# Kernel tuning notes

Measured on AMD Instinct MI355X. Metric: run time of the kernel, lower is better.

## Reference

```python
import jax, jax.numpy as jnp
import numpy as np

H = 1024  # hidden_size
B, S = 64, 2048


def setup_inputs() -> dict:
    key = jax.random.key(0)
    ks = jax.random.split(key, 9)
    d = {
        "s_t": jax.random.normal(ks[0], (B, 2 * H), jnp.float32),
        "h_i": jax.random.normal(ks[1], (B, S, 2 * H), jnp.float32),
        "coverage": jax.random.uniform(ks[2], (B, S), jnp.float32),
        # parameters (torch Linear: y = x @ W.T + b)
        "W_h": jax.random.normal(ks[3], (H, 2 * H), jnp.float32) / np.sqrt(2 * H),
        "b_h": jnp.zeros((H,), jnp.float32),
        "W_s": jax.random.normal(ks[4], (H, 2 * H), jnp.float32) / np.sqrt(2 * H),
        "b_s": jnp.zeros((H,), jnp.float32),
        "W_c": jax.random.normal(ks[5], (H, 1), jnp.float32),  # no bias
        "v_a": jax.random.normal(ks[6], (1, H), jnp.float32) / np.sqrt(H),
        "b_a": jnp.zeros((1,), jnp.float32),
    }
    return d


def reference(s_t, h_i, coverage, W_h, b_h, W_s, b_s, W_c, v_a, b_a):
    # Wi_hi: (B,S,H)
    Wi_hi = jnp.einsum("bsd,hd->bsh", h_i, W_h) + b_h
    # Ws_s: (B,H)
    Ws_s = jnp.einsum("bd,hd->bh", s_t, W_s) + b_s
    # coverage features: (B,S,H)  (W_c is (H,1))
    cov_feat = coverage[:, :, None] * W_c[:, 0]
    # scores: (B,S)
    E = jnp.einsum("bsh,h->bs", jnp.tanh(Wi_hi + Ws_s[:, None, :] + cov_feat), v_a[0]) + b_a[0]
    A = jax.nn.softmax(E, axis=-1)
    # context: (B,2H)
    C = jnp.einsum("bs,bsd->bd", A, h_i)
    new_cov = coverage + A
    return (C, A, new_cov)
```

## Files before the change

kernel.cpp:

```cpp
#include <hip/hip_runtime.h>
#include <hip/hip_bf16.h>

typedef __bf16 bf16x8_v __attribute__((ext_vector_type(8)));
typedef float  f32x4_v  __attribute__((ext_vector_type(4)));

static constexpr int kH = 1024;
static constexpr int kD = 2048;
static constexpr int kB = 64;
static constexpr int kS = 2048;
static constexpr int kM = kB * kS;

__device__ __forceinline__ void load_lds16(const void* g, void* l) {
  __builtin_amdgcn_global_load_lds(
      (const __attribute__((address_space(1))) unsigned int*)g,
      (__attribute__((address_space(3))) unsigned int*)l, 16, 0, 0);
}

__device__ __forceinline__ float fast_tanh(float x) {
  float e = __expf(2.0f * x);
  return 1.0f - 2.0f * __builtin_amdgcn_rcpf(e + 1.0f);
}

__global__ __launch_bounds__(256) void conv_tile_kernel(const float* __restrict__ in,
                                                        __bf16* __restrict__ out) {
  size_t g = (size_t)blockIdx.x * 256 + threadIdx.x;
  int p = (int)(g & 63);
  size_t tile = g >> 6;
  int kt = (int)(tile & 63);
  size_t mt16 = tile >> 6;
  int rr = p >> 2, s = p & 3;
  int c = s ^ ((rr >> 1) & 3);
  const float* src = in + (mt16 * 16 + rr) * (size_t)kD + kt * 32 + c * 8;
  float4 v0 = reinterpret_cast<const float4*>(src)[0];
  float4 v1 = reinterpret_cast<const float4*>(src)[1];
  bf16x8_v o = {(__bf16)v0.x, (__bf16)v0.y, (__bf16)v0.z, (__bf16)v0.w,
                (__bf16)v1.x, (__bf16)v1.y, (__bf16)v1.z, (__bf16)v1.w};
  reinterpret_cast<bf16x8_v*>(out)[g] = o;
}

__global__ __launch_bounds__(256) void prep_bias_kernel(
    const float* __restrict__ s_t, const float* __restrict__ W_s,
    const float* __restrict__ b_s, const float* __restrict__ b_h,
    float* __restrict__ biasBH) {
  int wave = blockIdx.x * 4 + (threadIdx.x >> 6);
  int lane = threadIdx.x & 63;
  int b = wave >> 10, h = wave & 1023;
  const float4* sp = reinterpret_cast<const float4*>(s_t + (size_t)b * kD);
  const float4* wp = reinterpret_cast<const float4*>(W_s + (size_t)h * kD);
  float acc = 0.f;
  for (int i = lane; i < kD / 4; i += 64) {
    float4 a = sp[i], w = wp[i];
    acc += a.x * w.x + a.y * w.y + a.z * w.z + a.w * w.w;
  }
  for (int m = 1; m < 64; m <<= 1) acc += __shfl_xor(acc, m);
  if (lane == 0) biasBH[wave] = acc + b_s[h] + b_h[h];
}

__global__ __launch_bounds__(512, 2) void gemm_score_kernel(
    const float* __restrict__ h_i,
    const __bf16* __restrict__ Wtl,
    const float* __restrict__ biasBH,
    const float* __restrict__ coverage,
    const float* __restrict__ Wc,
    const float* __restrict__ va,
    float* __restrict__ E) {
  const int bid = blockIdx.x;
  const int xcd = bid & 7;
  const int slot = bid >> 3;
  const int nblk = slot & 3;
  const int n0 = nblk * 256;
  const int m0 = (xcd * 64 + (slot >> 2)) * 256;

  const int tid = threadIdx.x;
  const int lane = tid & 63;
  const int wid = tid >> 6;
  const int wm = wid >> 2, wn = wid & 3;

  __shared__ char lds[2 * 32768];

  f32x4_v acc[8][4];
#pragma unroll
  for (int m = 0; m < 8; ++m)
#pragma unroll
    for (int n = 0; n < 4; ++n) acc[m][n] = {0.f, 0.f, 0.f, 0.f};

  const int l15 = lane & 15;
  const int j = lane >> 4;
  const int slot16 = (j ^ ((l15 >> 1) & 3)) << 4;

  const int arow = wid * 32 + (lane >> 1);
  const int ah = lane & 1;
  const float* Ag = h_i + (size_t)(m0 + arow) * kD + ah * 16;
  const int ast = arow >> 4;
  const int arr = arow & 15;
  const int ax = (arr >> 1) & 3;
  const int aw0 = ast * 1024 + arr * 64 + (((2 * ah) ^ ax) << 4);
  const int aw1 = ast * 1024 + arr * 64 + (((2 * ah + 1) ^ ax) << 4);

  const __bf16* Bsrc0 = Wtl + ((size_t)(nblk * 16 + wid * 2) * 64) * 512 + lane * 8;
  const __bf16* Bsrc1 = Wtl + ((size_t)(nblk * 16 + wid * 2 + 1) * 64) * 512 + lane * 8;

  f32x4_v avP[4], avQ[4];

#define LOADA(T, AV)                                                  \
  do {                                                                \
    const float* p_ = Ag + (size_t)(T) * 32;                          \
    AV[0] = *reinterpret_cast<const f32x4_v*>(p_);                    \
    AV[1] = *reinterpret_cast<const f32x4_v*>(p_ + 4);                \
    AV[2] = *reinterpret_cast<const f32x4_v*>(p_ + 8);                \
    AV[3] = *reinterpret_cast<const f32x4_v*>(p_ + 12);               \
  } while (0)

#define WRITEA(AV, B)                                                 \
  do {                                                                \
    char* base_ = lds + (B) * 32768;                                  \
    bf16x8_v o0_ = {(__bf16)AV[0][0], (__bf16)AV[0][1], (__bf16)AV[0][2], (__bf16)AV[0][3], \
                    (__bf16)AV[1][0], (__bf16)AV[1][1], (__bf16)AV[1][2], (__bf16)AV[1][3]}; \
    bf16x8_v o1_ = {(__bf16)AV[2][0], (__bf16)AV[2][1], (__bf16)AV[2][2], (__bf16)AV[2][3], \
                    (__bf16)AV[3][0], (__bf16)AV[3][1], (__bf16)AV[3][2], (__bf16)AV[3][3]}; \
    *reinterpret_cast<bf16x8_v*>(base_ + aw0) = o0_;                  \
    *reinterpret_cast<bf16x8_v*>(base_ + aw1) = o1_;                  \
  } while (0)

#define GLOADB(T, B)                                                  \
  do {                                                                \
    load_lds16(Bsrc0 + (size_t)(T) * 512, lds + (B) * 32768 + 16384 + (wid * 2) * 1024); \
    load_lds16(Bsrc1 + (size_t)(T) * 512, lds + (B) * 32768 + 16384 + (wid * 2 + 1) * 1024); \
  } while (0)

#define TILE(T, WAITN)                                                \
  do {                                                                \
    asm volatile("s_waitcnt vmcnt(" #WAITN ")" ::: "memory");         \
    __builtin_amdgcn_s_barrier();                                     \
    __builtin_amdgcn_sched_barrier(0);                                \
    const char* Ab_ = lds + ((T) & 1) * 32768;                        \
    const char* Bb_ = Ab_ + 16384;                                    \
    bf16x8_v b_[4], a_[4];                                            \
    _Pragma("unroll")                                                 \
    for (int n = 0; n < 4; ++n)                                       \
      b_[n] = *reinterpret_cast<const bf16x8_v*>(                     \
          Bb_ + (wn * 4 + n) * 1024 + l15 * 64 + slot16);             \
    _Pragma("unroll")                                                 \
    for (int mi = 0; mi < 4; ++mi)                                    \
      a_[mi] = *reinterpret_cast<const bf16x8_v*>(                    \
          Ab_ + (wm * 8 + mi) * 1024 + l15 * 64 + slot16);            \
    __builtin_amdgcn_s_setprio(1);                                    \
    _Pragma("unroll")                                                 \
    for (int mi = 0; mi < 4; ++mi)                                    \
      _Pragma("unroll")                                               \
      for (int n = 0; n < 4; ++n)                                     \
        acc[mi][n] = __builtin_amdgcn_mfma_f32_16x16x32_bf16(a_[mi], b_[n], acc[mi][n], 0, 0, 0); \
    __builtin_amdgcn_s_setprio(0);                                    \
    _Pragma("unroll")                                                 \
    for (int mi = 0; mi < 4; ++mi)                                    \
      a_[mi] = *reinterpret_cast<const bf16x8_v*>(                    \
          Ab_ + (wm * 8 + 4 + mi) * 1024 + l15 * 64 + slot16);        \
    __builtin_amdgcn_s_setprio(1);                                    \
    _Pragma("unroll")                                                 \
    for (int mi = 0; mi < 4; ++mi)                                    \
      _Pragma("unroll")                                               \
      for (int n = 0; n < 4; ++n)                                     \
        acc[4 + mi][n] = __builtin_amdgcn_mfma_f32_16x16x32_bf16(a_[mi], b_[n], acc[4 + mi][n], 0, 0, 0); \
    __builtin_amdgcn_s_setprio(0);                                    \
  } while (0)

#define POSTE(T, AV)                                                  \
  do {                                                                \
    WRITEA(AV, ((T) + 1) & 1);                   \
    asm volatile("s_waitcnt lgkmcnt(0)" ::: "memory");                \
    __builtin_amdgcn_s_barrier();                                     \
    __builtin_amdgcn_sched_barrier(0);                                \
    if ((T) + 2 < 64) GLOADB((T) + 2, (T) & 1);                       \
    if ((T) + 3 < 64) LOADA((T) + 3, AV);                             \
  } while (0)

  LOADA(0, avP);
  asm volatile("s_waitcnt vmcnt(0)" ::: "memory");
  WRITEA(avP, 0);
  GLOADB(0, 0);
  LOADA(1, avP);
  GLOADB(1, 1);
  LOADA(2, avQ);
  asm volatile("s_waitcnt lgkmcnt(0)" ::: "memory");
  __builtin_amdgcn_s_barrier();
  __builtin_amdgcn_sched_barrier(0);

  for (int t = 0; t < 62; t += 2) {
    TILE(t, 6);
    POSTE(t, avP);
    TILE(t + 1, 6);
    POSTE(t + 1, avQ);
  }
  TILE(62, 2);
  POSTE(62, avP);
  TILE(63, 0);

#undef LOADA
#undef WRITEA
#undef GLOADB
#undef TILE
#undef POSTE

  const int bb = m0 >> 11;
  const int colg = lane & 15;
  const int rowg = lane >> 4;
  float bias_v[4], wc_v[4], va_v[4];
#pragma unroll
  for (int n = 0; n < 4; ++n) {
    int h = n0 + wn * 64 + n * 16 + colg;
    bias_v[n] = biasBH[bb * kH + h];
    wc_v[n] = Wc[h];
    va_v[n] = va[h];
  }
  const int s_tile = (m0 & (kS - 1));
#pragma unroll
  for (int m = 0; m < 8; ++m) {
    int sbase = s_tile + wm * 128 + m * 16 + rowg * 4;
    float cov[4], rowsum[4];
#pragma unroll
    for (int q = 0; q < 4; ++q) {
      cov[q] = coverage[bb * kS + sbase + q];
      rowsum[q] = 0.f;
    }
#pragma unroll
    for (int n = 0; n < 4; ++n) {
#pragma unroll
      for (int q = 0; q < 4; ++q) {
        float z = acc[m][n][q] + bias_v[n] + cov[q] * wc_v[n];
        rowsum[q] += fast_tanh(z) * va_v[n];
      }
    }
#pragma unroll
    for (int q = 0; q < 4; ++q) {
      float v = rowsum[q];
      v += __shfl_xor(v, 1);
      v += __shfl_xor(v, 2);
      v += __shfl_xor(v, 4);
      v += __shfl_xor(v, 8);
      if (colg == 0) atomicAdd(&E[bb * kS + sbase + q], v);
    }
  }
}

__global__ __launch_bounds__(256) void softmax_kernel(
    const float* __restrict__ E, const float* __restrict__ coverage,
    float* __restrict__ A, float* __restrict__ newcov) {
  int b = blockIdx.x;
  int tid = threadIdx.x;
  int wid = tid >> 6, lane = tid & 63;
  __shared__ float wred[4];
  float ev[8];
  float mx = -INFINITY;
#pragma unroll
  for (int i = 0; i < 8; ++i) {
    ev[i] = E[b * kS + tid + i * 256];
    mx = fmaxf(mx, ev[i]);
  }
  for (int m = 1; m < 64; m <<= 1) mx = fmaxf(mx, __shfl_xor(mx, m));
  if (lane == 0) wred[wid] = mx;
  __syncthreads();
  mx = fmaxf(fmaxf(wred[0], wred[1]), fmaxf(wred[2], wred[3]));
  __syncthreads();
  float sum = 0.f;
#pragma unroll
  for (int i = 0; i < 8; ++i) {
    ev[i] = __expf(ev[i] - mx);
    sum += ev[i];
  }
  for (int m = 1; m < 64; m <<= 1) sum += __shfl_xor(sum, m);
  if (lane == 0) wred[wid] = sum;
  __syncthreads();
  sum = wred[0] + wred[1] + wred[2] + wred[3];
  float inv = 1.f / sum;
#pragma unroll
  for (int i = 0; i < 8; ++i) {
    int s = tid + i * 256;
    float a = ev[i] * inv;
    A[b * kS + s] = a;
    newcov[b * kS + s] = coverage[b * kS + s] + a;
  }
}

__global__ __launch_bounds__(256) void context_kernel(
    const float* __restrict__ h_i, const float* __restrict__ A,
    float* __restrict__ C) {
  int b = blockIdx.x;
  int d = blockIdx.y * 1024 + threadIdx.x * 4;
  int s0 = blockIdx.z * 256;
  const float* hp = h_i + ((size_t)b * kS + s0) * kD + d;
  const float* ap = A + b * kS + s0;
  float4 acc = {0.f, 0.f, 0.f, 0.f};
  for (int s = 0; s < 256; ++s) {
    float a = ap[s];
    float4 v = *reinterpret_cast<const float4*>(hp + (size_t)s * kD);
    acc.x += a * v.x;
    acc.y += a * v.y;
    acc.z += a * v.z;
    acc.w += a * v.w;
  }
  atomicAdd(&C[b * kD + d + 0], acc.x);
  atomicAdd(&C[b * kD + d + 1], acc.y);
  atomicAdd(&C[b * kD + d + 2], acc.z);
  atomicAdd(&C[b * kD + d + 3], acc.w);
}

extern "C" void kernel_launch(void* const* d_in, const int* in_sizes, int n_in,
                              void* d_out, int out_size, void* d_ws, size_t ws_size,
                              hipStream_t stream) {
  const float* s_t      = (const float*)d_in[0];
  const float* h_i      = (const float*)d_in[1];
  const float* coverage = (const float*)d_in[2];
  const float* W_h      = (const float*)d_in[3];
  const float* b_h      = (const float*)d_in[4];
  const float* W_s      = (const float*)d_in[5];
  const float* b_s      = (const float*)d_in[6];
  const float* W_c      = (const float*)d_in[7];
  const float* v_a      = (const float*)d_in[8];

  float* out = (float*)d_out;
  float* C      = out;
  float* A      = out + kB * kD;
  float* newcov = A + kB * kS;

  char* ws = (char*)d_ws;
  __bf16* Wtl   = (__bf16*)ws;
  float* biasBH = (float*)(ws + (4u << 20));
  float* E      = (float*)(ws + (4u << 20) + (256u << 10));

  hipMemsetAsync(E, 0, (size_t)kB * kS * sizeof(float), stream);
  hipMemsetAsync(C, 0, (size_t)kB * kD * sizeof(float), stream);

  conv_tile_kernel<<<kH, 256, 0, stream>>>(W_h, Wtl);
  prep_bias_kernel<<<(kB * kH) / 4, 256, 0, stream>>>(s_t, W_s, b_s, b_h, biasBH);

  gemm_score_kernel<<<2048, 512, 0, stream>>>(h_i, Wtl, biasBH, coverage,
                                              W_c, v_a, E);

  softmax_kernel<<<kB, 256, 0, stream>>>(E, coverage, A, newcov);

  dim3 gc(kB, kD / 1024, kS / 256);
  context_kernel<<<gc, 256, 0, stream>>>(h_i, A, C);
}
```

Measured before the change: 943.9 us.

## Triple-buffer B tiles and merge into a single barrier per K-step

Moves the GEMM main loop from a two-barrier double-buffered schedule to one barrier per K-tile. B tiles now rotate through three LDS buffers, and A keeps its two bf16 buffers, so prefetch for tile T+2 can be issued right after the barrier. The bf16 conversion and LDS write of the next A tile move to the end of each tile's MFMA work. LDS use per block grows from 64KB to 80KB, which may affect how many blocks fit per CU.

Result: faster. 916.5 us (-2.9%).

```diff
diff --git a/kernel.cpp b/kernel.cpp
--- a/kernel.cpp
+++ b/kernel.cpp
@@ -76,7 +76,7 @@
   const int wid = tid >> 6;
   const int wm = wid >> 2, wn = wid & 3;
 
-  __shared__ char lds[2 * 32768];
+  __shared__ __align__(16) char lds[81920];
 
   f32x4_v acc[8][4];
 #pragma unroll
@@ -111,9 +111,9 @@
     AV[3] = *reinterpret_cast<const f32x4_v*>(p_ + 12);               \
   } while (0)
 
-#define WRITEA(AV, B)                                                 \
+#define WRITEA(AV, BUF)                                               \
   do {                                                                \
-    char* base_ = lds + (B) * 32768;                                  \
+    char* base_ = lds + (BUF) * 16384;                                \
     bf16x8_v o0_ = {(__bf16)AV[0][0], (__bf16)AV[0][1], (__bf16)AV[0][2], (__bf16)AV[0][3], \
                     (__bf16)AV[1][0], (__bf16)AV[1][1], (__bf16)AV[1][2], (__bf16)AV[1][3]}; \
     bf16x8_v o1_ = {(__bf16)AV[2][0], (__bf16)AV[2][1], (__bf16)AV[2][2], (__bf16)AV[2][3], \
@@ -122,19 +122,25 @@
     *reinterpret_cast<bf16x8_v*>(base_ + aw1) = o1_;                  \
   } while (0)
 
-#define GLOADB(T, B)                                                  \
+#define GLOADB(T)                                                     \
   do {                                                                \
-    load_lds16(Bsrc0 + (size_t)(T) * 512, lds + (B) * 32768 + 16384 + (wid * 2) * 1024); \
-    load_lds16(Bsrc1 + (size_t)(T) * 512, lds + (B) * 32768 + 16384 + (wid * 2 + 1) * 1024); \
+    char* bd_ = lds + 32768 + ((T) % 3) * 16384;                      \
+    load_lds16(Bsrc0 + (size_t)(T) * 512, bd_ + (wid * 2) * 1024);    \
+    load_lds16(Bsrc1 + (size_t)(T) * 512, bd_ + (wid * 2 + 1) * 1024);\
   } while (0)
 
-#define TILE(T, WAITN)                                                \
+#define TILE13(T, AVC, AVN)                                           \
   do {                                                                \
-    asm volatile("s_waitcnt vmcnt(" #WAITN ")" ::: "memory");         \
+    asm volatile("s_waitcnt vmcnt(6)" ::: "memory");                  \
+    asm volatile("s_waitcnt lgkmcnt(0)" ::: "memory");                \
     __builtin_amdgcn_s_barrier();                                     \
     __builtin_amdgcn_sched_barrier(0);                                \
-    const char* Ab_ = lds + ((T) & 1) * 32768;                        \
-    const char* Bb_ = Ab_ + 16384;                                    \
+    if ((T) + 2 < 64) {                                               \
+      GLOADB((T) + 2);                                                \
+      LOADA((T) + 2, AVN);                                            \
+    }                                                                 \
+    const char* Ab_ = lds + ((T) & 1) * 16384;                        \
+    const char* Bb_ = lds + 32768 + ((T) % 3) * 16384;                \
     bf16x8_v b_[4], a_[4];                                            \
     _Pragma("unroll")                                                 \
     for (int n = 0; n < 4; ++n)                                       \
@@ -162,44 +168,25 @@
       for (int n = 0; n < 4; ++n)                                     \
         acc[4 + mi][n] = __builtin_amdgcn_mfma_f32_16x16x32_bf16(a_[mi], b_[n], acc[4 + mi][n], 0, 0, 0); \
     __builtin_amdgcn_s_setprio(0);                                    \
+    if ((T) + 1 < 64) WRITEA(AVC, ((T) + 1) & 1);                     \
   } while (0)
 
-#define POSTE(T, AV)                                                  \
-  do {                                                                \
-    WRITEA(AV, ((T) + 1) & 1);                   \
-    asm volatile("s_waitcnt lgkmcnt(0)" ::: "memory");                \
-    __builtin_amdgcn_s_barrier();                                     \
-    __builtin_amdgcn_sched_barrier(0);                                \
-    if ((T) + 2 < 64) GLOADB((T) + 2, (T) & 1);                       \
-    if ((T) + 3 < 64) LOADA((T) + 3, AV);                             \
-  } while (0)
-
+  GLOADB(0);
+  GLOADB(1);
   LOADA(0, avP);
   asm volatile("s_waitcnt vmcnt(0)" ::: "memory");
   WRITEA(avP, 0);
-  GLOADB(0, 0);
   LOADA(1, avP);
-  GLOADB(1, 1);
-  LOADA(2, avQ);
-  asm volatile("s_waitcnt lgkmcnt(0)" ::: "memory");
-  __builtin_amdgcn_s_barrier();
-  __builtin_amdgcn_sched_barrier(0);
-
-  for (int t = 0; t < 62; t += 2) {
-    TILE(t, 6);
-    POSTE(t, avP);
-    TILE(t + 1, 6);
-    POSTE(t + 1, avQ);
-  }
-  TILE(62, 2);
-  POSTE(62, avP);
-  TILE(63, 0);
+
+  for (int t = 0; t < 64; t += 2) {
+    TILE13(t, avP, avQ);
+    TILE13(t + 1, avQ, avP);
+  }
 
 #undef LOADA
 #undef WRITEA
 #undef GLOADB
-#undef TILE
-#undef POSTE
+#undef TILE13
 
   const int bb = m0 >> 11;
   const int colg = lane & 15;
```
